# Kernel tuning notes

Hardware: AMD Instinct MI355X
Metric: run time of the kernel (lower is better)

## Reference

```python
import jax, jax.numpy as jnp
import numpy as np

N_EMBED = 1024
N_HEADS = 16
CTX = 2048
B, T = 4, 2048
HD = N_EMBED // N_HEADS


def setup_inputs() -> dict:
    key = jax.random.key(0)
    ks = jax.random.split(key, 5)
    scale = 1.0 / np.sqrt(N_EMBED)
    return {
        "x": jax.random.normal(ks[0], (B, T, N_EMBED), dtype=jnp.float32),
        "wq": jax.random.normal(ks[1], (N_EMBED, N_EMBED), dtype=jnp.float32) * scale,
        "wk": jax.random.normal(ks[2], (N_EMBED, N_EMBED), dtype=jnp.float32) * scale,
        "wv": jax.random.normal(ks[3], (N_EMBED, N_EMBED), dtype=jnp.float32) * scale,
        "wo": jax.random.normal(ks[4], (N_EMBED, N_EMBED), dtype=jnp.float32) * scale,
    }


def reference(x, wq, wk, wv, wo):
    b, t, c = x.shape
    # nn.Linear applies x @ W.T ; split heads -> [B, H, T, hd]
    def proj(w):
        return jnp.einsum("btc,dc->btd", x, w).reshape(b, t, N_HEADS, HD).transpose(0, 2, 1, 3)
    q, k, v = proj(wq), proj(wk), proj(wv)
    scores = jnp.einsum("bhqd,bhkd->bhqk", q, k) * (HD ** -0.5)
    causal = jnp.tril(jnp.ones((t, t), dtype=bool))
    scores = jnp.where(causal[None, None, :, :], scores, -jnp.inf)
    a = jax.nn.softmax(scores, axis=-1)
    o = jnp.einsum("bhqk,bhkd->bhqd", a, v)  # [B,H,T,hd]
    o = o.transpose(0, 2, 1, 3).reshape(b, t, c)
    return jnp.einsum("btc,dc->btd", o, wo)
```

## Files before the change

kernel.cpp:

```cpp
#include <hip/hip_runtime.h>
#include <stdint.h>


typedef __attribute__((ext_vector_type(8))) short bf16x8;
typedef __attribute__((ext_vector_type(4))) float f32x4;
typedef unsigned short us;

#define LOG2E 1.4426950408889634f

#define GL2LDS16(g, l)                                                          \
  __builtin_amdgcn_global_load_lds(                                             \
      (const __attribute__((address_space(1))) unsigned int*)(g),               \
      (__attribute__((address_space(3))) unsigned int*)(l), 16, 0, 0)

__device__ inline us f2bf(float f) {
  union { float f; unsigned int u; } v; v.f = f;
  unsigned int u = v.u;
  u += 0x7FFFu + ((u >> 16) & 1u);
  return (us)(u >> 16);
}

__global__ void cast_f32_bf16(const float* __restrict__ in,
                              us* __restrict__ out, int n) {
  int i = (blockIdx.x * blockDim.x + threadIdx.x) * 8;
  if (i >= n) return;
  float4 a = *reinterpret_cast<const float4*>(in + i);
  float4 b = *reinterpret_cast<const float4*>(in + i + 4);
  union { us u[8]; uint4 v; } o;
  o.u[0] = f2bf(a.x); o.u[1] = f2bf(a.y); o.u[2] = f2bf(a.z); o.u[3] = f2bf(a.w);
  o.u[4] = f2bf(b.x); o.u[5] = f2bf(b.y); o.u[6] = f2bf(b.z); o.u[7] = f2bf(b.w);
  *reinterpret_cast<uint4*>(out + i) = o.v;
}

__global__ void cast4_w(const float* __restrict__ w0, const float* __restrict__ w1,
                        const float* __restrict__ w2, const float* __restrict__ w3,
                        us* __restrict__ out) {
  int i = (blockIdx.x * blockDim.x + threadIdx.x) * 8;
  int seg = i >> 20;
  const float* s = (seg == 0) ? w0 : (seg == 1) ? w1 : (seg == 2) ? w2 : w3;
  float sc = (seg == 0) ? (0.125f * LOG2E) : 1.0f;
  int off = i & ((1 << 20) - 1);
  float4 a = *reinterpret_cast<const float4*>(s + off);
  float4 b = *reinterpret_cast<const float4*>(s + off + 4);
  union { us u[8]; uint4 v; } o;
  o.u[0] = f2bf(a.x * sc); o.u[1] = f2bf(a.y * sc);
  o.u[2] = f2bf(a.z * sc); o.u[3] = f2bf(a.w * sc);
  o.u[4] = f2bf(b.x * sc); o.u[5] = f2bf(b.y * sc);
  o.u[6] = f2bf(b.z * sc); o.u[7] = f2bf(b.w * sc);
  *reinterpret_cast<uint4*>(out + i) = o.v;
}

template <int OUT_BF16>
__global__ __launch_bounds__(256, 2) void gemm_bt(
    const us* __restrict__ A, const us* __restrict__ Bw,
    void* __restrict__ Cv, int M, int N, int K) {
  __shared__ __align__(16) us Al[128 * 32];
  __shared__ __align__(16) us Bl[128 * 32];
  const int tid = threadIdx.x;
  const int lane = tid & 63;
  const int w = tid >> 6;
  const int quad = lane >> 4;
  const int l16 = lane & 15;
  const int m0 = blockIdx.y * 128;
  const int n0 = blockIdx.x * 128;
  const int wm = w >> 1, wn = w & 1;
  const int arow = lane >> 2;
  const int acol = (lane & 3) * 8;
  f32x4 acc[4][4] = {};

  for (int k0 = 0; k0 < K; k0 += 32) {
    __syncthreads();
    for (int c = 0; c < 2; ++c) {
      int chunk = 2 * w + c;
      int ldsoff = __builtin_amdgcn_readfirstlane(chunk * 512);
      GL2LDS16(A + (size_t)(m0 + chunk * 16 + arow) * K + k0 + acol, &Al[ldsoff]);
      GL2LDS16(Bw + (size_t)(n0 + chunk * 16 + arow) * K + k0 + acol, &Bl[ldsoff]);
    }
    __syncthreads();
    bf16x8 af[4], bfr[4];
#pragma unroll
    for (int mi = 0; mi < 4; ++mi)
      af[mi] = *reinterpret_cast<const bf16x8*>(&Al[(wm * 64 + mi * 16 + l16) * 32 + quad * 8]);
#pragma unroll
    for (int ni = 0; ni < 4; ++ni)
      bfr[ni] = *reinterpret_cast<const bf16x8*>(&Bl[(wn * 64 + ni * 16 + l16) * 32 + quad * 8]);
#pragma unroll
    for (int mi = 0; mi < 4; ++mi)
#pragma unroll
      for (int ni = 0; ni < 4; ++ni)
        acc[mi][ni] = __builtin_amdgcn_mfma_f32_16x16x32_bf16(af[mi], bfr[ni], acc[mi][ni], 0, 0, 0);
  }

#pragma unroll
  for (int mi = 0; mi < 4; ++mi)
#pragma unroll
    for (int ni = 0; ni < 4; ++ni)
#pragma unroll
      for (int r = 0; r < 4; ++r) {
        int row = m0 + wm * 64 + mi * 16 + quad * 4 + r;
        int col = n0 + wn * 64 + ni * 16 + l16;
        if (OUT_BF16)
          ((us*)Cv)[(size_t)row * N + col] = f2bf(acc[mi][ni][r]);
        else
          ((float*)Cv)[(size_t)row * N + col] = acc[mi][ni][r];
      }
}

__global__ __launch_bounds__(256) void transpose_v(const us* __restrict__ QKV,
                                                   us* __restrict__ Vt) {
  __shared__ __align__(16) us lds[64 * 80];
  const int bid = blockIdx.x;
  const int kt = bid & 31;
  const int bh = bid >> 5;
  const int b = bh >> 4, h = bh & 15;
  const int tid = threadIdx.x;
#pragma unroll
  for (int it = 0; it < 2; ++it) {
    int u = it * 256 + tid;
    int j = u >> 3;
    int dc = (u & 7) * 8;
    uint4 raw = *reinterpret_cast<const uint4*>(
        &QKV[((size_t)(b * 2048 + kt * 64 + j)) * 3072 + 2048 + h * 64 + dc]);
    us tmp[8];
    *reinterpret_cast<uint4*>(tmp) = raw;
    int sj = (j & 15) * 4 + (j >> 4);
#pragma unroll
    for (int e = 0; e < 8; ++e) lds[(dc + e) * 80 + sj] = tmp[e];
  }
  __syncthreads();
  int d = tid >> 2, c = tid & 3;
  size_t orow = ((size_t)(bh * 64 + d)) * 2048 + kt * 64 + c * 16;
  *reinterpret_cast<uint4*>(&Vt[orow]) = *reinterpret_cast<const uint4*>(&lds[d * 80 + c * 16]);
  *reinterpret_cast<uint4*>(&Vt[orow + 8]) = *reinterpret_cast<const uint4*>(&lds[d * 80 + c * 16 + 8]);
}

__global__ __launch_bounds__(256, 2) void attn(
    const us* __restrict__ QKV, const us* __restrict__ Vt,
    us* __restrict__ O) {
  __shared__ __align__(16) us Kl[64 * 64];
  __shared__ __align__(16) us Vl[64 * 64];
  __shared__ __align__(16) us Pl[4][32 * 64];
  const int bid = blockIdx.x;
  const int pr = bid & 7;
  const int h = (bid >> 3) & 15;
  const int b = bid >> 7;
  const int qtA = pr, qtB = 15 - pr;
  const int q0A = qtA * 128, q0B = qtB * 128;
  const int tid = threadIdx.x, lane = tid & 63, w = tid >> 6;
  const int quad = lane >> 4, l16 = lane & 15;
  const size_t rowbase = (size_t)b * 2048;
  const int qcol = h * 64;
  const int kcol = 1024 + h * 64;

  bf16x8 qfA[2][2], qfB[2][2];
#pragma unroll
  for (int qg = 0; qg < 2; ++qg)
#pragma unroll
    for (int dc = 0; dc < 2; ++dc) {
      qfA[qg][dc] = *reinterpret_cast<const bf16x8*>(
          &QKV[(rowbase + q0A + qg * 64 + w * 16 + l16) * 3072 + qcol + dc * 32 + quad * 8]);
      qfB[qg][dc] = *reinterpret_cast<const bf16x8*>(
          &QKV[(rowbase + q0B + qg * 64 + w * 16 + l16) * 3072 + qcol + dc * 32 + quad * 8]);
    }

  f32x4 oaccA[2][4] = {}, oaccB[2][4] = {};
  float lsumA[2][4] = {}, lsumB[2][4] = {};

  const int srow = lane >> 3;
  const int sunit = lane & 7;
  const int nA = qtA * 2 + 2;
  const int nB = qtB * 2 + 2;

  auto process = [&](int q0, bf16x8 (&qf)[2][2], f32x4 (&oacc)[2][4],
                     float (&lsum)[2][4], int kt) {
    f32x4 s[2][4] = {};
#pragma unroll
    for (int t = 0; t < 4; ++t) {
      int krow = t * 16 + l16;
#pragma unroll
      for (int dc = 0; dc < 2; ++dc) {
        bf16x8 kf = *reinterpret_cast<const bf16x8*>(
            &Kl[krow * 64 + (((dc * 4 + quad) ^ (l16 & 7)) * 8)]);
        s[0][t] = __builtin_amdgcn_mfma_f32_16x16x32_bf16(qf[0][dc], kf, s[0][t], 0, 0, 0);
        s[1][t] = __builtin_amdgcn_mfma_f32_16x16x32_bf16(qf[1][dc], kf, s[1][t], 0, 0, 0);
      }
    }
#pragma unroll
    for (int qg = 0; qg < 2; ++qg) {
      float p[4][4];
      bool do_mask = (kt * 64 + 63) > (q0 + qg * 64 + w * 16);
      if (do_mask) {
#pragma unroll
        for (int t = 0; t < 4; ++t)
#pragma unroll
          for (int r = 0; r < 4; ++r) {
            float e = exp2f(s[qg][t][r]);
            int kg = kt * 64 + t * 16 + l16;
            int qgl = q0 + qg * 64 + w * 16 + quad * 4 + r;
            p[t][r] = (kg <= qgl) ? e : 0.f;
            lsum[qg][r] += p[t][r];
          }
      } else {
#pragma unroll
        for (int t = 0; t < 4; ++t)
#pragma unroll
          for (int r = 0; r < 4; ++r) {
            float e = exp2f(s[qg][t][r]);
            p[t][r] = e;
            lsum[qg][r] += e;
          }
      }
#pragma unroll
      for (int r = 0; r < 4; ++r) {
        int prow = qg * 16 + quad * 4 + r;
        uint2 val;
        val.x = __builtin_amdgcn_perm(__float_as_uint(p[1][r]), __float_as_uint(p[0][r]), 0x07060302u);
        val.y = __builtin_amdgcn_perm(__float_as_uint(p[3][r]), __float_as_uint(p[2][r]), 0x07060302u);
        char* dst = (char*)&Pl[w][0] + prow * 128 +
                    (((l16 >> 1) ^ (prow & 7)) * 16) + (l16 & 1) * 8;
        *reinterpret_cast<uint2*>(dst) = val;
      }
    }
    asm volatile("s_waitcnt lgkmcnt(0)" ::: "memory");
#pragma unroll
    for (int kc = 0; kc < 2; ++kc) {
      bf16x8 pf[2];
#pragma unroll
      for (int qg = 0; qg < 2; ++qg)
        pf[qg] = *reinterpret_cast<const bf16x8*>(
            (const char*)&Pl[w][0] + (qg * 16 + l16) * 128 + (((kc * 4 + quad) ^ (l16 & 7)) * 16));
#pragma unroll
      for (int dt = 0; dt < 4; ++dt) {
        bf16x8 vf = *reinterpret_cast<const bf16x8*>(
            &Vl[(dt * 16 + l16) * 64 + (((kc * 4 + quad) ^ (l16 & 7)) * 8)]);
        oacc[0][dt] = __builtin_amdgcn_mfma_f32_16x16x32_bf16(pf[0], vf, oacc[0][dt], 0, 0, 0);
        oacc[1][dt] = __builtin_amdgcn_mfma_f32_16x16x32_bf16(pf[1], vf, oacc[1][dt], 0, 0, 0);
      }
    }
  };

  for (int kt = 0; kt < nB; ++kt) {
    __syncthreads();
#pragma unroll
    for (int c = 0; c < 2; ++c) {
      int rr = w * 16 + c * 8 + srow;
      int base = __builtin_amdgcn_readfirstlane((w * 16 + c * 8) * 64);
      int gu = sunit ^ (rr & 7);
      GL2LDS16(QKV + (rowbase + kt * 64 + rr) * 3072 + kcol + gu * 8, &Kl[base]);
      GL2LDS16(Vt + ((size_t)((b * 16 + h) * 64 + rr)) * 2048 + kt * 64 + gu * 8, &Vl[base]);
    }
    __syncthreads();
    process(q0B, qfB, oaccB, lsumB, kt);
    if (kt < nA) process(q0A, qfA, oaccA, lsumA, kt);
  }

  auto finalize = [&](int q0, f32x4 (&oacc)[2][4], float (&lsum)[2][4]) {
#pragma unroll
    for (int qg = 0; qg < 2; ++qg) {
      float inv[4];
#pragma unroll
      for (int r = 0; r < 4; ++r) {
        float v = lsum[qg][r];
        v += __shfl_xor(v, 1); v += __shfl_xor(v, 2);
        v += __shfl_xor(v, 4); v += __shfl_xor(v, 8);
        inv[r] = 1.0f / v;
      }
#pragma unroll
      for (int dt = 0; dt < 4; ++dt)
#pragma unroll
        for (int r = 0; r < 4; ++r) {
          int row = q0 + qg * 64 + w * 16 + quad * 4 + r;
          O[(rowbase + row) * 1024 + qcol + dt * 16 + l16] = f2bf(oacc[qg][dt][r] * inv[r]);
        }
    }
  };
  finalize(q0A, oaccA, lsumA);
  finalize(q0B, oaccB, lsumB);
}

extern "C" void kernel_launch(void* const* d_in, const int* in_sizes, int n_in,
                              void* d_out, int out_size, void* d_ws, size_t ws_size,
                              hipStream_t stream) {
  const float* x = (const float*)d_in[0];
  const float* wq = (const float*)d_in[1];
  const float* wk = (const float*)d_in[2];
  const float* wv = (const float*)d_in[3];
  const float* wo = (const float*)d_in[4];

  const int BT = 8192, E = 1024;
  const size_t NX = (size_t)BT * E;
  const size_t NW = (size_t)E * E;

  us* xb = (us*)d_ws;
  us* wbuf = xb + NX;
  us* QKV = wbuf + 4 * NW;
  us* VtB = QKV + (size_t)BT * 3 * E;
  us* Ob = xb;

  cast_f32_bf16<<<(int)(NX / 8 / 256), 256, 0, stream>>>(x, xb, (int)NX);
  cast4_w<<<(int)(4 * NW / 8 / 256), 256, 0, stream>>>(wq, wk, wv, wo, wbuf);

  gemm_bt<1><<<dim3(24, 64), 256, 0, stream>>>(xb, wbuf, QKV, BT, 3 * E, E);
  transpose_v<<<64 * 32, 256, 0, stream>>>(QKV, VtB);
  attn<<<4 * 16 * 8, 256, 0, stream>>>(QKV, VtB, Ob);
  gemm_bt<0><<<dim3(8, 64), 256, 0, stream>>>(Ob, wbuf + 3 * NW, (float*)d_out, BT, E, E);
}
```

Baseline: 272.1 us.

## Split attention q-rows over 8 waves and merge the cast kernels

The attention kernel now launches 512 threads per block. Each of the 8 waves owns 16 query rows per tile instead of 32, which halves per-wave accumulators and registers and aims for higher occupancy. A per-wave causal check skips K tiles that lie entirely beyond that wave's rows, and each thread issues one K/V load to LDS per tile. The x and weight cast kernels are fused into a single launch. The trade-off is less reuse of K/V fragments per wave, since each kf is used by one MFMA instead of two, and more LDS reads per MFMA.

```diff
diff --git a/kernel.cpp b/kernel.cpp
--- a/kernel.cpp
+++ b/kernel.cpp
@@ -20,34 +20,32 @@
   return (us)(u >> 16);
 }
 
-__global__ void cast_f32_bf16(const float* __restrict__ in,
-                              us* __restrict__ out, int n) {
+__global__ void cast_all(const float* __restrict__ x,
+                         const float* __restrict__ w0, const float* __restrict__ w1,
+                         const float* __restrict__ w2, const float* __restrict__ w3,
+                         us* __restrict__ xb, us* __restrict__ wbuf) {
   int i = (blockIdx.x * blockDim.x + threadIdx.x) * 8;
-  if (i >= n) return;
-  float4 a = *reinterpret_cast<const float4*>(in + i);
-  float4 b = *reinterpret_cast<const float4*>(in + i + 4);
-  union { us u[8]; uint4 v; } o;
-  o.u[0] = f2bf(a.x); o.u[1] = f2bf(a.y); o.u[2] = f2bf(a.z); o.u[3] = f2bf(a.w);
-  o.u[4] = f2bf(b.x); o.u[5] = f2bf(b.y); o.u[6] = f2bf(b.z); o.u[7] = f2bf(b.w);
-  *reinterpret_cast<uint4*>(out + i) = o.v;
-}
-
-__global__ void cast4_w(const float* __restrict__ w0, const float* __restrict__ w1,
-                        const float* __restrict__ w2, const float* __restrict__ w3,
-                        us* __restrict__ out) {
-  int i = (blockIdx.x * blockDim.x + threadIdx.x) * 8;
-  int seg = i >> 20;
-  const float* s = (seg == 0) ? w0 : (seg == 1) ? w1 : (seg == 2) ? w2 : w3;
-  float sc = (seg == 0) ? (0.125f * LOG2E) : 1.0f;
-  int off = i & ((1 << 20) - 1);
-  float4 a = *reinterpret_cast<const float4*>(s + off);
-  float4 b = *reinterpret_cast<const float4*>(s + off + 4);
+  const float* src;
+  us* dst;
+  float sc = 1.0f;
+  if (i < (8 << 20)) {
+    src = x + i; dst = xb + i;
+  } else {
+    int j = i - (8 << 20);
+    int seg = j >> 20;
+    int off = j & ((1 << 20) - 1);
+    const float* w = (seg == 0) ? w0 : (seg == 1) ? w1 : (seg == 2) ? w2 : w3;
+    if (seg == 0) sc = 0.125f * LOG2E;
+    src = w + off; dst = wbuf + j;
+  }
+  float4 a = *reinterpret_cast<const float4*>(src);
+  float4 b = *reinterpret_cast<const float4*>(src + 4);
   union { us u[8]; uint4 v; } o;
   o.u[0] = f2bf(a.x * sc); o.u[1] = f2bf(a.y * sc);
   o.u[2] = f2bf(a.z * sc); o.u[3] = f2bf(a.w * sc);
   o.u[4] = f2bf(b.x * sc); o.u[5] = f2bf(b.y * sc);
   o.u[6] = f2bf(b.z * sc); o.u[7] = f2bf(b.w * sc);
-  *reinterpret_cast<uint4*>(out + i) = o.v;
+  *reinterpret_cast<uint4*>(dst) = o.v;
 }
 
 template <int OUT_BF16>
@@ -134,46 +132,43 @@
   *reinterpret_cast<uint4*>(&Vt[orow + 8]) = *reinterpret_cast<const uint4*>(&lds[d * 80 + c * 16 + 8]);
 }
 
-__global__ __launch_bounds__(256, 2) void attn(
+__global__ __launch_bounds__(512, 4) void attn(
     const us* __restrict__ QKV, const us* __restrict__ Vt,
     us* __restrict__ O) {
   __shared__ __align__(16) us Kl[64 * 64];
   __shared__ __align__(16) us Vl[64 * 64];
-  __shared__ __align__(16) us Pl[4][32 * 64];
+  __shared__ __align__(16) us Pl[8][16 * 64];
   const int bid = blockIdx.x;
   const int pr = bid & 7;
   const int h = (bid >> 3) & 15;
   const int b = bid >> 7;
-  const int qtA = pr, qtB = 15 - pr;
-  const int q0A = qtA * 128, q0B = qtB * 128;
+  const int q0A = pr * 128, q0B = (15 - pr) * 128;
   const int tid = threadIdx.x, lane = tid & 63, w = tid >> 6;
   const int quad = lane >> 4, l16 = lane & 15;
   const size_t rowbase = (size_t)b * 2048;
   const int qcol = h * 64;
   const int kcol = 1024 + h * 64;
 
-  bf16x8 qfA[2][2], qfB[2][2];
-#pragma unroll
-  for (int qg = 0; qg < 2; ++qg)
-#pragma unroll
-    for (int dc = 0; dc < 2; ++dc) {
-      qfA[qg][dc] = *reinterpret_cast<const bf16x8*>(
-          &QKV[(rowbase + q0A + qg * 64 + w * 16 + l16) * 3072 + qcol + dc * 32 + quad * 8]);
-      qfB[qg][dc] = *reinterpret_cast<const bf16x8*>(
-          &QKV[(rowbase + q0B + qg * 64 + w * 16 + l16) * 3072 + qcol + dc * 32 + quad * 8]);
-    }
-
-  f32x4 oaccA[2][4] = {}, oaccB[2][4] = {};
-  float lsumA[2][4] = {}, lsumB[2][4] = {};
-
-  const int srow = lane >> 3;
-  const int sunit = lane & 7;
-  const int nA = qtA * 2 + 2;
-  const int nB = qtB * 2 + 2;
-
-  auto process = [&](int q0, bf16x8 (&qf)[2][2], f32x4 (&oacc)[2][4],
-                     float (&lsum)[2][4], int kt) {
-    f32x4 s[2][4] = {};
+  bf16x8 qfA[2], qfB[2];
+#pragma unroll
+  for (int dc = 0; dc < 2; ++dc) {
+    qfA[dc] = *reinterpret_cast<const bf16x8*>(
+        &QKV[(rowbase + q0A + w * 16 + l16) * 3072 + qcol + dc * 32 + quad * 8]);
+    qfB[dc] = *reinterpret_cast<const bf16x8*>(
+        &QKV[(rowbase + q0B + w * 16 + l16) * 3072 + qcol + dc * 32 + quad * 8]);
+  }
+
+  f32x4 oaccA[4] = {}, oaccB[4] = {};
+  float lsumA[4] = {}, lsumB[4] = {};
+
+  const int rr = tid >> 3;
+  const int gu = (tid & 7) ^ (rr & 7);
+  const int base = __builtin_amdgcn_readfirstlane(w * 512);
+  const int nB = 2 * (15 - pr) + 2;
+
+  auto process = [&](int q0, bf16x8 (&qf)[2], f32x4 (&oacc)[4],
+                     float (&lsum)[4], int kt) {
+    f32x4 s[4] = {};
 #pragma unroll
     for (int t = 0; t < 4; ++t) {
       int krow = t * 16 + l16;
@@ -181,98 +176,81 @@
       for (int dc = 0; dc < 2; ++dc) {
         bf16x8 kf = *reinterpret_cast<const bf16x8*>(
             &Kl[krow * 64 + (((dc * 4 + quad) ^ (l16 & 7)) * 8)]);
-        s[0][t] = __builtin_amdgcn_mfma_f32_16x16x32_bf16(qf[0][dc], kf, s[0][t], 0, 0, 0);
-        s[1][t] = __builtin_amdgcn_mfma_f32_16x16x32_bf16(qf[1][dc], kf, s[1][t], 0, 0, 0);
-      }
-    }
-#pragma unroll
-    for (int qg = 0; qg < 2; ++qg) {
-      float p[4][4];
-      bool do_mask = (kt * 64 + 63) > (q0 + qg * 64 + w * 16);
-      if (do_mask) {
-#pragma unroll
-        for (int t = 0; t < 4; ++t)
-#pragma unroll
-          for (int r = 0; r < 4; ++r) {
-            float e = exp2f(s[qg][t][r]);
-            int kg = kt * 64 + t * 16 + l16;
-            int qgl = q0 + qg * 64 + w * 16 + quad * 4 + r;
-            p[t][r] = (kg <= qgl) ? e : 0.f;
-            lsum[qg][r] += p[t][r];
-          }
-      } else {
-#pragma unroll
-        for (int t = 0; t < 4; ++t)
-#pragma unroll
-          for (int r = 0; r < 4; ++r) {
-            float e = exp2f(s[qg][t][r]);
-            p[t][r] = e;
-            lsum[qg][r] += e;
-          }
-      }
-#pragma unroll
-      for (int r = 0; r < 4; ++r) {
-        int prow = qg * 16 + quad * 4 + r;
-        uint2 val;
-        val.x = __builtin_amdgcn_perm(__float_as_uint(p[1][r]), __float_as_uint(p[0][r]), 0x07060302u);
-        val.y = __builtin_amdgcn_perm(__float_as_uint(p[3][r]), __float_as_uint(p[2][r]), 0x07060302u);
-        char* dst = (char*)&Pl[w][0] + prow * 128 +
-                    (((l16 >> 1) ^ (prow & 7)) * 16) + (l16 & 1) * 8;
-        *reinterpret_cast<uint2*>(dst) = val;
-      }
+        s[t] = __builtin_amdgcn_mfma_f32_16x16x32_bf16(qf[dc], kf, s[t], 0, 0, 0);
+      }
+    }
+    float p[4][4];
+    bool do_mask = (kt * 64 + 63) > (q0 + w * 16);
+    if (do_mask) {
+#pragma unroll
+      for (int t = 0; t < 4; ++t)
+#pragma unroll
+        for (int r = 0; r < 4; ++r) {
+          float e = exp2f(s[t][r]);
+          int kg = kt * 64 + t * 16 + l16;
+          int qgl = q0 + w * 16 + quad * 4 + r;
+          p[t][r] = (kg <= qgl) ? e : 0.f;
+          lsum[r] += p[t][r];
+        }
+    } else {
+#pragma unroll
+      for (int t = 0; t < 4; ++t)
+#pragma unroll
+        for (int r = 0; r < 4; ++r) {
+          float e = exp2f(s[t][r]);
+          p[t][r] = e;
+          lsum[r] += e;
+        }
+    }
+#pragma unroll
+    for (int r = 0; r < 4; ++r) {
+      int prow = quad * 4 + r;
+      uint2 val;
+      val.x = __builtin_amdgcn_perm(__float_as_uint(p[1][r]), __float_as_uint(p[0][r]), 0x07060302u);
+      val.y = __builtin_amdgcn_perm(__float_as_uint(p[3][r]), __float_as_uint(p[2][r]), 0x07060302u);
+      char* dst = (char*)&Pl[w][0] + prow * 128 +
+                  (((l16 >> 1) ^ (prow & 7)) * 16) + (l16 & 1) * 8;
+      *reinterpret_cast<uint2*>(dst) = val;
     }
     asm volatile("s_waitcnt lgkmcnt(0)" ::: "memory");
 #pragma unroll
     for (int kc = 0; kc < 2; ++kc) {
-      bf16x8 pf[2];
-#pragma unroll
-      for (int qg = 0; qg < 2; ++qg)
-        pf[qg] = *reinterpret_cast<const bf16x8*>(
-            (const char*)&Pl[w][0] + (qg * 16 + l16) * 128 + (((kc * 4 + quad) ^ (l16 & 7)) * 16));
+      bf16x8 pf = *reinterpret_cast<const bf16x8*>(
+          (const char*)&Pl[w][0] + l16 * 128 + (((kc * 4 + quad) ^ (l16 & 7)) * 16));
 #pragma unroll
       for (int dt = 0; dt < 4; ++dt) {
         bf16x8 vf = *reinterpret_cast<const bf16x8*>(
             &Vl[(dt * 16 + l16) * 64 + (((kc * 4 + quad) ^ (l16 & 7)) * 8)]);
-        oacc[0][dt] = __builtin_amdgcn_mfma_f32_16x16x32_bf16(pf[0], vf, oacc[0][dt], 0, 0, 0);
-        oacc[1][dt] = __builtin_amdgcn_mfma_f32_16x16x32_bf16(pf[1], vf, oacc[1][dt], 0, 0, 0);
+        oacc[dt] = __builtin_amdgcn_mfma_f32_16x16x32_bf16(pf, vf, oacc[dt], 0, 0, 0);
       }
     }
   };
 
   for (int kt = 0; kt < nB; ++kt) {
     __syncthreads();
-#pragma unroll
-    for (int c = 0; c < 2; ++c) {
-      int rr = w * 16 + c * 8 + srow;
-      int base = __builtin_amdgcn_readfirstlane((w * 16 + c * 8) * 64);
-      int gu = sunit ^ (rr & 7);
-      GL2LDS16(QKV + (rowbase + kt * 64 + rr) * 3072 + kcol + gu * 8, &Kl[base]);
-      GL2LDS16(Vt + ((size_t)((b * 16 + h) * 64 + rr)) * 2048 + kt * 64 + gu * 8, &Vl[base]);
-    }
-    __syncthreads();
-    process(q0B, qfB, oaccB, lsumB, kt);
-    if (kt < nA) process(q0A, qfA, oaccA, lsumA, kt);
-  }
-
-  auto finalize = [&](int q0, f32x4 (&oacc)[2][4], float (&lsum)[2][4]) {
-#pragma unroll
-    for (int qg = 0; qg < 2; ++qg) {
-      float inv[4];
+    GL2LDS16(QKV + (rowbase + kt * 64 + rr) * 3072 + kcol + gu * 8, &Kl[base]);
+    GL2LDS16(Vt + ((size_t)((b * 16 + h) * 64 + rr)) * 2048 + kt * 64 + gu * 8, &Vl[base]);
+    __syncthreads();
+    if (kt * 64 <= q0B + w * 16 + 15) process(q0B, qfB, oaccB, lsumB, kt);
+    if (kt * 64 <= q0A + w * 16 + 15) process(q0A, qfA, oaccA, lsumA, kt);
+  }
+
+  auto finalize = [&](int q0, f32x4 (&oacc)[4], float (&lsum)[4]) {
+    float inv[4];
+#pragma unroll
+    for (int r = 0; r < 4; ++r) {
+      float v = lsum[r];
+      v += __shfl_xor(v, 1); v += __shfl_xor(v, 2);
+      v += __shfl_xor(v, 4); v += __shfl_xor(v, 8);
+      inv[r] = 1.0f / v;
+    }
+#pragma unroll
+    for (int dt = 0; dt < 4; ++dt)
 #pragma unroll
       for (int r = 0; r < 4; ++r) {
-        float v = lsum[qg][r];
-        v += __shfl_xor(v, 1); v += __shfl_xor(v, 2);
-        v += __shfl_xor(v, 4); v += __shfl_xor(v, 8);
-        inv[r] = 1.0f / v;
-      }
-#pragma unroll
-      for (int dt = 0; dt < 4; ++dt)
-#pragma unroll
-        for (int r = 0; r < 4; ++r) {
-          int row = q0 + qg * 64 + w * 16 + quad * 4 + r;
-          O[(rowbase + row) * 1024 + qcol + dt * 16 + l16] = f2bf(oacc[qg][dt][r] * inv[r]);
-        }
-    }
+        int row = q0 + w * 16 + quad * 4 + r;
+        O[(rowbase + row) * 1024 + qcol + dt * 16 + l16] = f2bf(oacc[dt][r] * inv[r]);
+      }
   };
   finalize(q0A, oaccA, lsumA);
   finalize(q0B, oaccB, lsumB);
@@ -297,11 +275,10 @@
   us* VtB = QKV + (size_t)BT * 3 * E;
   us* Ob = xb;
 
-  cast_f32_bf16<<<(int)(NX / 8 / 256), 256, 0, stream>>>(x, xb, (int)NX);
-  cast4_w<<<(int)(4 * NW / 8 / 256), 256, 0, stream>>>(wq, wk, wv, wo, wbuf);
+  cast_all<<<(int)((NX + 4 * NW) / 8 / 256), 256, 0, stream>>>(x, wq, wk, wv, wo, xb, wbuf);
 
   gemm_bt<1><<<dim3(24, 64), 256, 0, stream>>>(xb, wbuf, QKV, BT, 3 * E, E);
   transpose_v<<<64 * 32, 256, 0, stream>>>(QKV, VtB);
-  attn<<<4 * 16 * 8, 256, 0, stream>>>(QKV, VtB, Ob);
+  attn<<<4 * 16 * 8, 512, 0, stream>>>(QKV, VtB, Ob);
   gemm_bt<0><<<dim3(8, 64), 256, 0, stream>>>(Ob, wbuf + 3 * NW, (float*)d_out, BT, E, E);
 }
```

Result: faster. 261.7 us (-3.8%).
